# Kernel tuning notes

Hardware: AMD Instinct MI355X
Metric: run time of the kernel (lower is better)

Reference implementation:

```python
import jax, jax.numpy as jnp
import numpy as np

B, N, F, C = 8, 4096, 128, 128
EDGE_PROB = 0.01
NEG_INF = -1e9


def setup_inputs() -> dict:
    key = jax.random.key(0)
    k_x, k_a, k_w, k_s, k_d = jax.random.split(key, 5)
    x = jax.random.normal(k_x, (B, N, F), dtype=jnp.float32)
    A = (jax.random.uniform(k_a, (N, N)) < EDGE_PROB).astype(jnp.float32)
    A = jnp.maximum(A, jnp.eye(N, dtype=jnp.float32))
    W = jax.random.normal(k_w, (F, C), dtype=jnp.float32) * (1.0 / np.sqrt(F))
    b = jnp.zeros((C,), dtype=jnp.float32)
    a_src = jax.random.normal(k_s, (C,), dtype=jnp.float32) * 0.1
    a_dst = jax.random.normal(k_d, (C,), dtype=jnp.float32) * 0.1
    return {"x": x, "A": A, "W": W, "b": b, "a_src": a_src, "a_dst": a_dst}


def reference(x, A, W, b, a_src, a_dst):
    # GATConv (Spektral, dense mode, 1 head, activation=None) + outer LeakyReLU(0.3)
    h = jnp.einsum("bnf,fc->bnc", x, W)                      # [B,N,C]
    e_src = jnp.einsum("bnc,c->bn", h, a_src)                 # per-target logit
    e_dst = jnp.einsum("bnc,c->bn", h, a_dst)                 # per-source logit
    logits = jax.nn.leaky_relu(e_src[:, :, None] + e_dst[:, None, :], 0.2)  # [B,N,N]
    mask = jnp.where(A > 0, 0.0, NEG_INF)                     # [N,N], broadcast over batch
    alpha = jax.nn.softmax(logits + mask, axis=-1)            # masked softmax over neighbors
    out = jnp.einsum("bij,bjc->bic", alpha, h) + b            # neighbor aggregation + bias
    return jax.nn.leaky_relu(out, 0.3)
```

## Files before the change

kernel.cpp:

```cpp
#include <hip/hip_runtime.h>
#include <hip/hip_bf16.h>

#define N_NODES 4096
#define BATCH 8
#define FEAT 128
#define CAP 256

typedef float v2f __attribute__((ext_vector_type(2)));
typedef short short8 __attribute__((ext_vector_type(8)));
typedef float f32x4 __attribute__((ext_vector_type(4)));

__device__ __forceinline__ unsigned short f2bf(float f) {
    unsigned int u = __float_as_uint(f);
    u += 0x7fffu + ((u >> 16) & 1u);
    return (unsigned short)(u >> 16);
}

__device__ __forceinline__ unsigned int pk2bf(float a, float b) {
    return (unsigned int)f2bf(a) | ((unsigned int)f2bf(b) << 16);
}

__device__ __forceinline__ void fma8v(v2f* acc, v2f pp, uint4 hv) {
    unsigned int u;
    v2f t;
    u = hv.x; t[0] = __uint_as_float(u << 16); t[1] = __uint_as_float(u & 0xffff0000u);
    acc[0] += pp * t;
    u = hv.y; t[0] = __uint_as_float(u << 16); t[1] = __uint_as_float(u & 0xffff0000u);
    acc[1] += pp * t;
    u = hv.z; t[0] = __uint_as_float(u << 16); t[1] = __uint_as_float(u & 0xffff0000u);
    acc[2] += pp * t;
    u = hv.w; t[0] = __uint_as_float(u << 16); t[1] = __uint_as_float(u & 0xffff0000u);
    acc[3] += pp * t;
}

__global__ __launch_bounds__(512) void scan_k(const float* __restrict__ A,
                                              const float* __restrict__ W,
                                              unsigned short* __restrict__ nbr,
                                              int* __restrict__ deg,
                                              unsigned short* __restrict__ Wt) {
    __shared__ unsigned short seg[8 * 64];
    __shared__ int scnt[8];

    int tid = threadIdx.x;
    int lane = tid & 63;
    int w = tid >> 6;
    int i = blockIdx.x;

    {
        const float4* ar = (const float4*)(A + (size_t)i * N_NODES);
        unsigned long long below = (1ull << lane) - 1ull;
        float4 v0 = ar[w * 128 + lane];
        float4 v1 = ar[w * 128 + 64 + lane];
        int cnt = 0;
#define SCAN4(vv, base)                                                         \
        {                                                                       \
            bool f0 = vv.x > 0.f, f1 = vv.y > 0.f, f2 = vv.z > 0.f, f3 = vv.w > 0.f; \
            unsigned long long m0 = __ballot(f0), m1 = __ballot(f1),            \
                               m2 = __ballot(f2), m3 = __ballot(f3);            \
            int pos = cnt + (int)__popcll(m0 & below) + (int)__popcll(m1 & below) \
                          + (int)__popcll(m2 & below) + (int)__popcll(m3 & below); \
            int colb = base;                                                    \
            if (f0) { if (pos < 64) seg[w * 64 + pos] = (unsigned short)(colb);     ++pos; } \
            if (f1) { if (pos < 64) seg[w * 64 + pos] = (unsigned short)(colb + 1); ++pos; } \
            if (f2) { if (pos < 64) seg[w * 64 + pos] = (unsigned short)(colb + 2); ++pos; } \
            if (f3) { if (pos < 64) seg[w * 64 + pos] = (unsigned short)(colb + 3); ++pos; } \
            cnt += (int)__popcll(m0) + (int)__popcll(m1)                        \
                 + (int)__popcll(m2) + (int)__popcll(m3);                       \
        }
        SCAN4(v0, 4 * (w * 128 + lane))
        SCAN4(v1, 4 * (w * 128 + 64 + lane))
#undef SCAN4
        if (lane == 0) scnt[w] = cnt < 64 ? cnt : 64;
    }
    __syncthreads();

    {
        int off = 0, d = 0;
#pragma unroll
        for (int t = 0; t < 8; ++t) {
            int c = scnt[t];
            if (t < w) off += c;
            d += c;
        }
        int cw = scnt[w];
        unsigned short* lst = nbr + (size_t)i * CAP;
        if (lane < cw && off + lane < CAP) lst[off + lane] = seg[w * 64 + lane];
        if (tid == 0) deg[i] = d < CAP ? d : CAP;
    }

    if (i == 0) {
        for (int e = tid; e < FEAT * FEAT; e += 512) {
            int k = e >> 7, n = e & 127;
            Wt[n * FEAT + k] = f2bf(W[e]);
        }
    }
}

__global__ __launch_bounds__(256) void gemm_mfma(const float* __restrict__ x,
                                                 const unsigned short* __restrict__ Wt,
                                                 const float* __restrict__ a_src,
                                                 const float* __restrict__ a_dst,
                                                 unsigned short* __restrict__ h,
                                                 float* __restrict__ es,
                                                 float* __restrict__ ed) {
    __shared__ unsigned short xs[64 * FEAT];
    __shared__ unsigned short wsh[FEAT * FEAT];

    int tid = threadIdx.x;
    int lane = tid & 63;
    int w = tid >> 6;
    int ln = lane & 15;
    int kg = lane >> 4;
    int m0 = blockIdx.x * 64;

#pragma unroll
    for (int it = 0; it < 16; ++it) {
        int idx = it * 256 + tid;
        int n = idx >> 5, c = idx & 31;
        uint2 v = *(const uint2*)(Wt + (size_t)n * FEAT + c * 4);
        int kb = (c * 8) ^ ((n & 7) << 4);
        *(uint2*)((char*)wsh + n * 256 + kb) = v;
    }
#pragma unroll
    for (int it = 0; it < 8; ++it) {
        int idx = it * 256 + tid;
        int r = idx >> 5, c = idx & 31;
        float4 v = *(const float4*)(x + (size_t)(m0 + r) * FEAT + c * 4);
        uint2 p; p.x = pk2bf(v.x, v.y); p.y = pk2bf(v.z, v.w);
        int kb = (c * 8) ^ ((r & 7) << 4);
        *(uint2*)((char*)xs + r * 256 + kb) = p;
    }
    __syncthreads();

    union frag { short8 s; uint u[4]; };
    int sw = (ln & 7) << 4;

    f32x4 acc[8];
#pragma unroll
    for (int t = 0; t < 8; ++t) acc[t] = (f32x4)(0.f);

    int ra = w * 16 + ln;
#pragma unroll
    for (int ks = 0; ks < 4; ++ks) {
        int klo = (ks * 64 + kg * 8) ^ sw;
        int khi = (ks * 64 + 32 + kg * 8) ^ sw;
        frag af;
        {
            uint2 lo = *(const uint2*)((const char*)xs + ra * 256 + klo);
            uint2 hi = *(const uint2*)((const char*)xs + ra * 256 + khi);
            af.u[0] = lo.x; af.u[1] = lo.y; af.u[2] = hi.x; af.u[3] = hi.y;
        }
#pragma unroll
        for (int t = 0; t < 8; ++t) {
            int n = t * 16 + ln;
            frag bf;
            uint2 lo = *(const uint2*)((const char*)wsh + n * 256 + klo);
            uint2 hi = *(const uint2*)((const char*)wsh + n * 256 + khi);
            bf.u[0] = lo.x; bf.u[1] = lo.y; bf.u[2] = hi.x; bf.u[3] = hi.y;
            acc[t] = __builtin_amdgcn_mfma_f32_16x16x32_bf16(af.s, bf.s, acc[t], 0, 0, 0);
        }
    }

    float as8[8], ad8[8];
#pragma unroll
    for (int t = 0; t < 8; ++t) { as8[t] = a_src[t * 16 + ln]; ad8[t] = a_dst[t * 16 + ln]; }

#pragma unroll
    for (int r = 0; r < 4; ++r) {
        int m = m0 + w * 16 + kg * 4 + r;
        float ps = 0.f, pd = 0.f;
#pragma unroll
        for (int t = 0; t < 8; ++t) {
            float vv = acc[t][r];
            h[(size_t)m * FEAT + t * 16 + ln] = f2bf(vv);
            ps += vv * as8[t];
            pd += vv * ad8[t];
        }
#pragma unroll
        for (int off = 8; off >= 1; off >>= 1) {
            ps += __shfl_xor(ps, off);
            pd += __shfl_xor(pd, off);
        }
        if (ln == 0) { es[m] = ps; ed[m] = pd; }
    }
}

__global__ __launch_bounds__(256) void aggregate(const unsigned short* __restrict__ h,
                                                 const float* __restrict__ es,
                                                 const float* __restrict__ ed,
                                                 const unsigned short* __restrict__ nbr,
                                                 const int* __restrict__ deg,
                                                 const float* __restrict__ bias,
                                                 float* __restrict__ out) {
    int lane = threadIdx.x & 63;
    int g = lane >> 4;
    int c8 = (lane & 15) * 8;
    int b = blockIdx.x & 7;
    int i = (blockIdx.x >> 3) * 4 + (threadIdx.x >> 6);

    int d = deg[i];
    const unsigned short* lst = nbr + (size_t)i * CAP;
    float esv = es[b * N_NODES + i];
    const float* edb = ed + b * N_NODES;

    float zv0 = -1e30f, zv1 = -1e30f, zv2 = -1e30f, zv3 = -1e30f;
    int cv0 = 0, cv1 = 0, cv2 = 0, cv3 = 0;
    float m = -1e30f;
#define PASS1(c, zz, cc)                                            \
    if (c * 64 < d) {                                               \
        int j = c * 64 + lane;                                      \
        if (j < d) {                                                \
            cc = lst[j];                                            \
            float z0 = esv + edb[cc];                               \
            zz = z0 > 0.f ? z0 : 0.2f * z0;                         \
        }                                                           \
        m = fmaxf(m, zz);                                           \
    }
    PASS1(0, zv0, cv0)
    PASS1(1, zv1, cv1)
    PASS1(2, zv2, cv2)
    PASS1(3, zv3, cv3)
#undef PASS1
#pragma unroll
    for (int off = 32; off >= 1; off >>= 1) m = fmaxf(m, __shfl_xor(m, off));

    const unsigned short* hb = h + (size_t)b * N_NODES * FEAT;
    v2f acc0[4], acc1[4];
#pragma unroll
    for (int k = 0; k < 4; ++k) { acc0[k] = (v2f)(0.f); acc1[k] = (v2f)(0.f); }
    float s = 0.f;
#define PASS2(c, zz, cc)                                                        \
    if (c * 64 < d) {                                                           \
        float p = __expf(zz - m);                                               \
        s += p;                                                                 \
        int n = d - c * 64; if (n > 64) n = 64;                                 \
        int nn = (n + 7) & ~7;                                                  \
        for (int jj = 0; jj < nn; jj += 8) {                                    \
            int j0 = jj + g, j1 = jj + 4 + g;                                   \
            float p0 = __shfl(p, j0); int cj0 = __shfl(cc, j0);                 \
            float p1 = __shfl(p, j1); int cj1 = __shfl(cc, j1);                 \
            uint4 h0 = *(const uint4*)(hb + (size_t)cj0 * FEAT + c8);           \
            uint4 h1 = *(const uint4*)(hb + (size_t)cj1 * FEAT + c8);           \
            v2f pp0; pp0[0] = p0; pp0[1] = p0;                                  \
            v2f pp1; pp1[0] = p1; pp1[1] = p1;                                  \
            fma8v(acc0, pp0, h0);                                               \
            fma8v(acc1, pp1, h1);                                               \
        }                                                                       \
    }
    PASS2(0, zv0, cv0)
    PASS2(1, zv1, cv1)
    PASS2(2, zv2, cv2)
    PASS2(3, zv3, cv3)
#undef PASS2

#pragma unroll
    for (int off = 32; off >= 1; off >>= 1) s += __shfl_xor(s, off);
    float inv = 1.0f / s;

#pragma unroll
    for (int k = 0; k < 4; ++k) acc0[k] += acc1[k];
#pragma unroll
    for (int k = 0; k < 4; ++k) {
        acc0[k][0] += __shfl_xor(acc0[k][0], 16);
        acc0[k][1] += __shfl_xor(acc0[k][1], 16);
        acc0[k][0] += __shfl_xor(acc0[k][0], 32);
        acc0[k][1] += __shfl_xor(acc0[k][1], 32);
    }

    if (lane < 16) {
        float4 b0 = *(const float4*)(bias + c8);
        float4 b1 = *(const float4*)(bias + c8 + 4);
        float o[8];
        o[0] = acc0[0][0] * inv + b0.x; o[1] = acc0[0][1] * inv + b0.y;
        o[2] = acc0[1][0] * inv + b0.z; o[3] = acc0[1][1] * inv + b0.w;
        o[4] = acc0[2][0] * inv + b1.x; o[5] = acc0[2][1] * inv + b1.y;
        o[6] = acc0[3][0] * inv + b1.z; o[7] = acc0[3][1] * inv + b1.w;
#pragma unroll
        for (int k = 0; k < 8; ++k) o[k] = o[k] > 0.f ? o[k] : 0.3f * o[k];
        float* orow = out + ((size_t)b * N_NODES + i) * FEAT + c8;
        *(float4*)orow = make_float4(o[0], o[1], o[2], o[3]);
        *(float4*)(orow + 4) = make_float4(o[4], o[5], o[6], o[7]);
    }
}

extern "C" void kernel_launch(void* const* d_in, const int* in_sizes, int n_in,
                              void* d_out, int out_size, void* d_ws, size_t ws_size,
                              hipStream_t stream) {
    const float* x     = (const float*)d_in[0];
    const float* A     = (const float*)d_in[1];
    const float* W     = (const float*)d_in[2];
    const float* bias  = (const float*)d_in[3];
    const float* a_src = (const float*)d_in[4];
    const float* a_dst = (const float*)d_in[5];
    float* out = (float*)d_out;

    char* ws = (char*)d_ws;
    unsigned short* h  = (unsigned short*)ws;
    float* es = (float*)(h + (size_t)BATCH * N_NODES * FEAT);
    float* ed = es + BATCH * N_NODES;
    unsigned short* Wt = (unsigned short*)(ed + BATCH * N_NODES);
    int* dg = (int*)(Wt + FEAT * FEAT);
    unsigned short* nb = (unsigned short*)(dg + N_NODES);

    hipLaunchKernelGGL(scan_k, dim3(N_NODES), dim3(512), 0, stream,
                       A, W, nb, dg, Wt);
    hipLaunchKernelGGL(gemm_mfma, dim3(BATCH * N_NODES / 64), dim3(256), 0, stream,
                       x, Wt, a_src, a_dst, h, es, ed);
    hipLaunchKernelGGL(aggregate, dim3(BATCH * N_NODES / 4), dim3(256), 0, stream,
                       h, es, ed, nb, dg, bias, out);
}
```

Before: 59.68 us.

## Scan adjacency rows with one wave per four rows and register prefetch

The adjacency scan now gives each wavefront four whole rows and walks all 4096 columns in 16 chunks. It prefetches the next chunk into registers and writes neighbor indices straight to global memory, with no LDS staging and no block barrier. The grid shrinks from 4096 blocks to 256 blocks of 256 threads, which also lifts the old per-wave cap of 64 neighbors. This removes cross-wave synchronization and gives more memory-level parallelism per wave, but it may under-fill the GPU with only 1024 waves and serial chunk loops.

```diff
diff --git a/kernel.cpp b/kernel.cpp
--- a/kernel.cpp
+++ b/kernel.cpp
@@ -33,63 +33,70 @@
     acc[3] += pp * t;
 }
 
-__global__ __launch_bounds__(512) void scan_k(const float* __restrict__ A,
+__global__ __launch_bounds__(256) void scan_k(const float* __restrict__ A,
                                               const float* __restrict__ W,
                                               unsigned short* __restrict__ nbr,
                                               int* __restrict__ deg,
                                               unsigned short* __restrict__ Wt) {
-    __shared__ unsigned short seg[8 * 64];
-    __shared__ int scnt[8];
-
     int tid = threadIdx.x;
     int lane = tid & 63;
     int w = tid >> 6;
-    int i = blockIdx.x;
-
-    {
-        const float4* ar = (const float4*)(A + (size_t)i * N_NODES);
-        unsigned long long below = (1ull << lane) - 1ull;
-        float4 v0 = ar[w * 128 + lane];
-        float4 v1 = ar[w * 128 + 64 + lane];
-        int cnt = 0;
-#define SCAN4(vv, base)                                                         \
-        {                                                                       \
-            bool f0 = vv.x > 0.f, f1 = vv.y > 0.f, f2 = vv.z > 0.f, f3 = vv.w > 0.f; \
-            unsigned long long m0 = __ballot(f0), m1 = __ballot(f1),            \
-                               m2 = __ballot(f2), m3 = __ballot(f3);            \
-            int pos = cnt + (int)__popcll(m0 & below) + (int)__popcll(m1 & below) \
-                          + (int)__popcll(m2 & below) + (int)__popcll(m3 & below); \
-            int colb = base;                                                    \
-            if (f0) { if (pos < 64) seg[w * 64 + pos] = (unsigned short)(colb);     ++pos; } \
-            if (f1) { if (pos < 64) seg[w * 64 + pos] = (unsigned short)(colb + 1); ++pos; } \
-            if (f2) { if (pos < 64) seg[w * 64 + pos] = (unsigned short)(colb + 2); ++pos; } \
-            if (f3) { if (pos < 64) seg[w * 64 + pos] = (unsigned short)(colb + 3); ++pos; } \
-            cnt += (int)__popcll(m0) + (int)__popcll(m1)                        \
-                 + (int)__popcll(m2) + (int)__popcll(m3);                       \
-        }
-        SCAN4(v0, 4 * (w * 128 + lane))
-        SCAN4(v1, 4 * (w * 128 + 64 + lane))
+    int r0 = blockIdx.x * 16 + w * 4;
+
+    const float4* a0 = (const float4*)(A + (size_t)(r0 + 0) * N_NODES);
+    const float4* a1 = (const float4*)(A + (size_t)(r0 + 1) * N_NODES);
+    const float4* a2 = (const float4*)(A + (size_t)(r0 + 2) * N_NODES);
+    const float4* a3 = (const float4*)(A + (size_t)(r0 + 3) * N_NODES);
+    unsigned short* l0 = nbr + (size_t)(r0 + 0) * CAP;
+    unsigned short* l1 = nbr + (size_t)(r0 + 1) * CAP;
+    unsigned short* l2 = nbr + (size_t)(r0 + 2) * CAP;
+    unsigned short* l3 = nbr + (size_t)(r0 + 3) * CAP;
+
+    unsigned long long below = (1ull << lane) - 1ull;
+    int c0 = 0, c1 = 0, c2 = 0, c3 = 0;
+
+    float4 u0 = a0[lane], u1 = a1[lane], u2 = a2[lane], u3 = a3[lane];
+
+#define SCAN4(vv, lst, cnt, base)                                               \
+    {                                                                           \
+        bool f0 = vv.x > 0.f, f1 = vv.y > 0.f, f2 = vv.z > 0.f, f3 = vv.w > 0.f; \
+        unsigned long long m0 = __ballot(f0), m1 = __ballot(f1),                \
+                           m2 = __ballot(f2), m3 = __ballot(f3);                \
+        int pos = cnt + (int)__popcll(m0 & below) + (int)__popcll(m1 & below)   \
+                      + (int)__popcll(m2 & below) + (int)__popcll(m3 & below);  \
+        int colb = base;                                                        \
+        if (f0) { if (pos < CAP) lst[pos] = (unsigned short)(colb);     ++pos; } \
+        if (f1) { if (pos < CAP) lst[pos] = (unsigned short)(colb + 1); ++pos; } \
+        if (f2) { if (pos < CAP) lst[pos] = (unsigned short)(colb + 2); ++pos; } \
+        if (f3) { if (pos < CAP) lst[pos] = (unsigned short)(colb + 3); ++pos; } \
+        cnt += (int)__popcll(m0) + (int)__popcll(m1)                            \
+             + (int)__popcll(m2) + (int)__popcll(m3);                           \
+    }
+
+    for (int c = 0; c < 16; ++c) {
+        float4 n0, n1, n2, n3;
+        if (c < 15) {
+            int idx = (c + 1) * 64 + lane;
+            n0 = a0[idx]; n1 = a1[idx]; n2 = a2[idx]; n3 = a3[idx];
+        }
+        int base = 4 * (c * 64 + lane);
+        SCAN4(u0, l0, c0, base)
+        SCAN4(u1, l1, c1, base)
+        SCAN4(u2, l2, c2, base)
+        SCAN4(u3, l3, c3, base)
+        u0 = n0; u1 = n1; u2 = n2; u3 = n3;
+    }
 #undef SCAN4
-        if (lane == 0) scnt[w] = cnt < 64 ? cnt : 64;
-    }
-    __syncthreads();
-
-    {
-        int off = 0, d = 0;
-#pragma unroll
-        for (int t = 0; t < 8; ++t) {
-            int c = scnt[t];
-            if (t < w) off += c;
-            d += c;
-        }
-        int cw = scnt[w];
-        unsigned short* lst = nbr + (size_t)i * CAP;
-        if (lane < cw && off + lane < CAP) lst[off + lane] = seg[w * 64 + lane];
-        if (tid == 0) deg[i] = d < CAP ? d : CAP;
-    }
-
-    if (i == 0) {
-        for (int e = tid; e < FEAT * FEAT; e += 512) {
+
+    if (lane == 0) {
+        deg[r0 + 0] = c0 < CAP ? c0 : CAP;
+        deg[r0 + 1] = c1 < CAP ? c1 : CAP;
+        deg[r0 + 2] = c2 < CAP ? c2 : CAP;
+        deg[r0 + 3] = c3 < CAP ? c3 : CAP;
+    }
+
+    if (blockIdx.x == 0) {
+        for (int e = tid; e < FEAT * FEAT; e += 256) {
             int k = e >> 7, n = e & 127;
             Wt[n * FEAT + k] = f2bf(W[e]);
         }
@@ -302,7 +309,7 @@
     int* dg = (int*)(Wt + FEAT * FEAT);
     unsigned short* nb = (unsigned short*)(dg + N_NODES);
 
-    hipLaunchKernelGGL(scan_k, dim3(N_NODES), dim3(512), 0, stream,
+    hipLaunchKernelGGL(scan_k, dim3(N_NODES / 16), dim3(256), 0, stream,
                        A, W, nb, dg, Wt);
     hipLaunchKernelGGL(gemm_mfma, dim3(BATCH * N_NODES / 64), dim3(256), 0, stream,
                        x, Wt, a_src, a_dst, h, es, ed);
```

Result: slower. 72.53 us (+21.5%).

## Split adjacency scan into bitmask pass and per-row wave list build

Applied to the files above, without the earlier changes.

Replaces the single per-row ballot-based neighbor scan with two kernels: a grid-stride pass that packs the dense float adjacency into a bitmask, then a one-wave-per-row kernel that prefix-sums popcounts and emits neighbor indices with ctz loops. The aim is a simpler, more bandwidth-friendly streaming read of the 64 MB adjacency and cheaper list construction. It adds an extra kernel launch and a 2 MB mask round trip through memory. The old per-wave 64-entry segment truncation is removed.

```diff
diff --git a/kernel.cpp b/kernel.cpp
--- a/kernel.cpp
+++ b/kernel.cpp
@@ -33,67 +33,61 @@
     acc[3] += pp * t;
 }
 
-__global__ __launch_bounds__(512) void scan_k(const float* __restrict__ A,
-                                              const float* __restrict__ W,
-                                              unsigned short* __restrict__ nbr,
-                                              int* __restrict__ deg,
-                                              unsigned short* __restrict__ Wt) {
-    __shared__ unsigned short seg[8 * 64];
-    __shared__ int scnt[8];
-
+__global__ __launch_bounds__(256) void bitscan(const float* __restrict__ A,
+                                               unsigned char* __restrict__ mask,
+                                               const float* __restrict__ W,
+                                               unsigned short* __restrict__ Wt) {
+    int tid = threadIdx.x;
+    const int nb = N_NODES * N_NODES / 8;
+    for (int t = blockIdx.x * 256 + tid; t < nb; t += gridDim.x * 256) {
+        const float4* p = (const float4*)(A + (size_t)t * 8);
+        float4 v0 = p[0], v1 = p[1];
+        unsigned int b = 0;
+        b |= (v0.x > 0.f) ? 1u : 0u;
+        b |= (v0.y > 0.f) ? 2u : 0u;
+        b |= (v0.z > 0.f) ? 4u : 0u;
+        b |= (v0.w > 0.f) ? 8u : 0u;
+        b |= (v1.x > 0.f) ? 16u : 0u;
+        b |= (v1.y > 0.f) ? 32u : 0u;
+        b |= (v1.z > 0.f) ? 64u : 0u;
+        b |= (v1.w > 0.f) ? 128u : 0u;
+        mask[t] = (unsigned char)b;
+    }
+    if (blockIdx.x == 0) {
+        for (int e = tid; e < FEAT * FEAT; e += 256) {
+            int k = e >> 7, n = e & 127;
+            Wt[n * FEAT + k] = f2bf(W[e]);
+        }
+    }
+}
+
+__global__ __launch_bounds__(256) void listbuild(const unsigned char* __restrict__ mask,
+                                                 unsigned short* __restrict__ nbr,
+                                                 int* __restrict__ deg) {
     int tid = threadIdx.x;
     int lane = tid & 63;
-    int w = tid >> 6;
-    int i = blockIdx.x;
-
-    {
-        const float4* ar = (const float4*)(A + (size_t)i * N_NODES);
-        unsigned long long below = (1ull << lane) - 1ull;
-        float4 v0 = ar[w * 128 + lane];
-        float4 v1 = ar[w * 128 + 64 + lane];
-        int cnt = 0;
-#define SCAN4(vv, base)                                                         \
-        {                                                                       \
-            bool f0 = vv.x > 0.f, f1 = vv.y > 0.f, f2 = vv.z > 0.f, f3 = vv.w > 0.f; \
-            unsigned long long m0 = __ballot(f0), m1 = __ballot(f1),            \
-                               m2 = __ballot(f2), m3 = __ballot(f3);            \
-            int pos = cnt + (int)__popcll(m0 & below) + (int)__popcll(m1 & below) \
-                          + (int)__popcll(m2 & below) + (int)__popcll(m3 & below); \
-            int colb = base;                                                    \
-            if (f0) { if (pos < 64) seg[w * 64 + pos] = (unsigned short)(colb);     ++pos; } \
-            if (f1) { if (pos < 64) seg[w * 64 + pos] = (unsigned short)(colb + 1); ++pos; } \
-            if (f2) { if (pos < 64) seg[w * 64 + pos] = (unsigned short)(colb + 2); ++pos; } \
-            if (f3) { if (pos < 64) seg[w * 64 + pos] = (unsigned short)(colb + 3); ++pos; } \
-            cnt += (int)__popcll(m0) + (int)__popcll(m1)                        \
-                 + (int)__popcll(m2) + (int)__popcll(m3);                       \
-        }
-        SCAN4(v0, 4 * (w * 128 + lane))
-        SCAN4(v1, 4 * (w * 128 + 64 + lane))
-#undef SCAN4
-        if (lane == 0) scnt[w] = cnt < 64 ? cnt : 64;
-    }
-    __syncthreads();
-
-    {
-        int off = 0, d = 0;
-#pragma unroll
-        for (int t = 0; t < 8; ++t) {
-            int c = scnt[t];
-            if (t < w) off += c;
-            d += c;
-        }
-        int cw = scnt[w];
-        unsigned short* lst = nbr + (size_t)i * CAP;
-        if (lane < cw && off + lane < CAP) lst[off + lane] = seg[w * 64 + lane];
-        if (tid == 0) deg[i] = d < CAP ? d : CAP;
-    }
-
-    if (i == 0) {
-        for (int e = tid; e < FEAT * FEAT; e += 512) {
-            int k = e >> 7, n = e & 127;
-            Wt[n * FEAT + k] = f2bf(W[e]);
-        }
-    }
+    int row = blockIdx.x * 4 + (tid >> 6);
+
+    unsigned long long bits = ((const unsigned long long*)mask)[(size_t)row * 64 + lane];
+    int pc = (int)__popcll(bits);
+    int pre = pc;
+#pragma unroll
+    for (int off = 1; off < 64; off <<= 1) {
+        int v = __shfl_up(pre, off);
+        if (lane >= off) pre += v;
+    }
+    int total = __shfl(pre, 63);
+    int pos = pre - pc;
+    unsigned short* lst = nbr + (size_t)row * CAP;
+    unsigned long long b = bits;
+    int colbase = lane << 6;
+    while (b) {
+        int j = __builtin_ctzll(b);
+        b &= b - 1;
+        if (pos < CAP) lst[pos] = (unsigned short)(colbase + j);
+        ++pos;
+    }
+    if (lane == 0) deg[row] = total < CAP ? total : CAP;
 }
 
 __global__ __launch_bounds__(256) void gemm_mfma(const float* __restrict__ x,
@@ -301,9 +295,10 @@
     unsigned short* Wt = (unsigned short*)(ed + BATCH * N_NODES);
     int* dg = (int*)(Wt + FEAT * FEAT);
     unsigned short* nb = (unsigned short*)(dg + N_NODES);
-
-    hipLaunchKernelGGL(scan_k, dim3(N_NODES), dim3(512), 0, stream,
-                       A, W, nb, dg, Wt);
+    unsigned char* mk = (unsigned char*)(nb + (size_t)N_NODES * CAP);
+
+    hipLaunchKernelGGL(bitscan, dim3(2048), dim3(256), 0, stream, A, mk, W, Wt);
+    hipLaunchKernelGGL(listbuild, dim3(N_NODES / 4), dim3(256), 0, stream, mk, nb, dg);
     hipLaunchKernelGGL(gemm_mfma, dim3(BATCH * N_NODES / 64), dim3(256), 0, stream,
                        x, Wt, a_src, a_dst, h, es, ed);
     hipLaunchKernelGGL(aggregate, dim3(BATCH * N_NODES / 4), dim3(256), 0, stream,
```

Result: slower. 67.56 us (+13.2%).
